# Optimization experiments

Hardware: AMD Instinct MI355X
Metric: run time of the kernel (lower is better)

## Reference

```python
import jax, jax.numpy as jnp
import numpy as np

K = 5  # Chebyshev order


def laplacian(w):
    # normalized Laplacian: I - D^{-1/2} W D^{-1/2}
    d = jnp.sum(w, axis=1)
    d_re = 1.0 / jnp.sqrt(d + 1e-5)
    return jnp.eye(w.shape[0], dtype=w.dtype) - d_re[:, None] * w * d_re[None, :]


def cheb_terms(x, lap, k):
    # x: [B,N,C], lap: [N,N] -> [B,k,N,C]
    # Faithful to torch code: T0 = ones, then (x, lap@x) recurrence for k>2.
    t0 = jnp.ones_like(x)
    if k == 1:
        return t0[:, None]
    t1 = jnp.matmul(lap, x)
    if k == 2:
        return jnp.stack([t0, t1], axis=1)
    terms = [t0, x, t1]
    tkm1, tk = x, t1
    for _ in range(3, k):
        tkm1, tk = tk, 2.0 * jnp.matmul(lap, tk) - tkm1
        terms.append(tk)
    return jnp.stack(terms, axis=1)


def graph_conv(x, lap, w, k):
    # torch: cp.permute(0,2,3,1).flatten(2) @ w, i.e. flat index = c*k + t
    t = cheb_terms(x, lap, k)                       # [B,k,N,C]
    C = x.shape[-1]
    O = w.shape[-1]
    return jnp.einsum('bknc,cko->bno', t, w.reshape(C, k, O))


def setup_inputs() -> dict:
    key = jax.random.key(0)
    ks = jax.random.split(key, 9)
    B, N, Cin, H = 8192, 32, 60, 128
    return {
        'x': jax.random.normal(ks[0], (B, N, Cin), dtype=jnp.float32),
        'adj': jax.random.normal(ks[1], (N, N), dtype=jnp.float32) * 0.1,
        'adj_bias': jax.random.normal(ks[2], (1,), dtype=jnp.float32) * 0.1 + 0.2,
        'w1': jax.random.normal(ks[3], (K * Cin, H), dtype=jnp.float32) * 0.05,
        'b1': jax.random.normal(ks[4], (1, 1, H), dtype=jnp.float32) * 0.05,
        'w2': jax.random.normal(ks[5], (K * H, H), dtype=jnp.float32) * 0.05,
        'b2': jax.random.normal(ks[6], (1, 1, H), dtype=jnp.float32) * 0.05,
        'fc_w': jax.random.normal(ks[7], (2, N * H), dtype=jnp.float32) * 0.02,
        'fc_b': jax.random.normal(ks[8], (2,), dtype=jnp.float32) * 0.02,
    }


def reference(x, adj, adj_bias, w1, b1, w2, b2, fc_w, fc_b):
    # DGCNN.forward (eval mode: dropout = identity)
    a = jax.nn.relu(adj + adj_bias)
    lap = laplacian(a)
    h = graph_conv(x, lap, w1, K)
    h = jax.nn.relu(h + b1)      # B1ReLU
    h = graph_conv(h, lap, w2, K)
    h = jax.nn.relu(h + b2)
    h = h.reshape(h.shape[0], -1)  # [B, N*H]
    return h @ fc_w.T + fc_b
```

## Files before the change

### kernel.cpp

```cpp
#include <hip/hip_runtime.h>

typedef unsigned short u16;
typedef unsigned int u32;
typedef short bf16x8 __attribute__((ext_vector_type(8)));
typedef float f32x4 __attribute__((ext_vector_type(4)));

#define MFMA16(a, b, c) __builtin_amdgcn_mfma_f32_16x16x32_bf16((a), (b), (c), 0, 0, 0)

__device__ __forceinline__ u16 f2bf(float f) {
  u32 u = __builtin_bit_cast(u32, f);
  u += 0x7FFFu + ((u >> 16) & 1u);
  return (u16)(u >> 16);
}
__device__ __forceinline__ u32 pk2bf(float a, float b) {
#if __has_builtin(__builtin_amdgcn_cvt_pk_bf16_f32)
  auto v = __builtin_amdgcn_cvt_pk_bf16_f32(a, b);
  return __builtin_bit_cast(u32, v);
#else
  return (u32)f2bf(a) | ((u32)f2bf(b) << 16);
#endif
}

#define WS_MGF   0
#define WS_WT1F  8192
#define WS_WT2F  73728
#define WS_B1    204800
#define WS_B2    205312

__global__ void prep_kernel(const float* __restrict__ adj,
                            const float* __restrict__ adj_bias,
                            const float* __restrict__ w1,
                            const float* __restrict__ b1,
                            const float* __restrict__ w2,
                            const float* __restrict__ b2,
                            char* __restrict__ ws) {
  const int tid = threadIdx.x;
  if (blockIdx.x == 0) {
    __shared__ float sa[1024], Ls[1024], L2s[1024], L3s[1024], sdre[32];
    float bias = adj_bias[0];
    for (int i = tid; i < 1024; i += 256) sa[i] = fmaxf(adj[i] + bias, 0.0f);
    __syncthreads();
    if (tid < 32) {
      float s = 0.0f;
      for (int c = 0; c < 32; ++c) s += sa[tid * 32 + c];
      sdre[tid] = 1.0f / sqrtf(s + 1e-5f);
    }
    __syncthreads();
    for (int i = tid; i < 1024; i += 256) {
      int n = i >> 5, c = i & 31;
      Ls[i] = (n == c ? 1.0f : 0.0f) - sdre[n] * sa[i] * sdre[c];
    }
    __syncthreads();
    for (int i = tid; i < 1024; i += 256) {
      int r = i >> 5, c = i & 31;
      float s = 0.0f;
      for (int m = 0; m < 32; ++m) s += Ls[r * 32 + m] * Ls[m * 32 + c];
      L2s[i] = s;
    }
    __syncthreads();
    for (int i = tid; i < 1024; i += 256) {
      int r = i >> 5, c = i & 31;
      float s = 0.0f;
      for (int m = 0; m < 32; ++m) s += L2s[r * 32 + m] * Ls[m * 32 + c];
      L3s[i] = s;
    }
    __syncthreads();
    u16* MGf = (u16*)(ws + WS_MGF);
    for (int i = tid; i < 4096; i += 256) {
      int jt = i >> 9, lane = (i >> 3) & 63, j = i & 7;
      int col = jt * 16 + (lane & 15);
      int k = ((lane >> 4) << 3) + j;
      int kk = col >> 5, np = col & 31;
      float v;
      if (kk == 0)      v = (np == k) ? 1.0f : 0.0f;
      else if (kk == 1) v = Ls[np * 32 + k];
      else if (kk == 2) v = 2.0f * L2s[np * 32 + k] - (np == k ? 1.0f : 0.0f);
      else              v = 4.0f * L3s[np * 32 + k] - 3.0f * Ls[np * 32 + k];
      MGf[i] = f2bf(v);
    }
    float* B1 = (float*)(ws + WS_B1);
    float* B2 = (float*)(ws + WS_B2);
    if (tid < 128) {
      float s = b1[tid];
      for (int c = 0; c < 60; ++c) s += w1[(c * 5) * 128 + tid];
      B1[tid] = s;
    } else {
      int o = tid - 128;
      float s = b2[o];
      for (int c = 0; c < 128; ++c) s += w2[(c * 5) * 128 + o];
      B2[o] = s;
    }
  } else {
    u16* WT1F = (u16*)(ws + WS_WT1F);
    u16* WT2F = (u16*)(ws + WS_WT2F);
    int g = (blockIdx.x - 1) * 256 + tid;
    for (int i = g; i < 32768; i += 16 * 256) {
      int ot = i >> 12, ks = (i >> 9) & 7, lane = (i >> 3) & 63, j = i & 7;
      int o = ot * 16 + (lane & 15);
      int kc = ks * 32 + ((lane >> 4) << 3) + j;
      int k = kc >> 6, c = kc & 63;
      WT1F[i] = (c < 60) ? f2bf(w1[(c * 5 + k + 1) * 128 + o]) : (u16)0;
    }
    for (int i = g; i < 65536; i += 16 * 256) {
      int mt = i >> 13, h = (i >> 12) & 1, ks = (i >> 9) & 7;
      int lane = (i >> 3) & 63, j = i & 7;
      int kc = ((ks >> 1) << 7) + ((ks & 1) << 5) + (h << 6) + (((lane >> 4)) << 3) + j;
      int k = kc >> 7, c = kc & 127;
      int o = (mt << 4) + (lane & 15);
      WT2F[i] = f2bf(w2[(c * 5 + k + 1) * 128 + o]);
    }
  }
}

__global__ __launch_bounds__(256, 3) void dgcnn_kernel(
    const float* __restrict__ x,
    const char* __restrict__ ws,
    const float* __restrict__ fc_w,
    const float* __restrict__ fc_b,
    float* __restrict__ out) {
  __shared__ __align__(16) char arena[52224];
  __shared__ float red[16];
  u16* XtA = (u16*)arena;
  u16* XtB = (u16*)(arena + 5120);
  u16* HtA = (u16*)arena;
  u16* HtB = (u16*)(arena + 9216);
  u16* YA  = (u16*)(arena + 18432);
  u16* YB  = (u16*)(arena + 35328);

  const u16* MGf  = (const u16*)(ws + WS_MGF);
  const u16* WT1F = (const u16*)(ws + WS_WT1F);
  const u16* WT2F = (const u16*)(ws + WS_WT2F);
  const float* bias1 = (const float*)(ws + WS_B1);
  const float* bias2 = (const float*)(ws + WS_B2);

  const int tid = threadIdx.x;
  const int w = tid >> 6, lane = tid & 63;
  const int l15 = lane & 15, q = lane >> 4;
  const int b0 = blockIdx.x * 2;
  const f32x4 z4 = {0.0f, 0.0f, 0.0f, 0.0f};

  bf16x8 mB0 = *(const bf16x8*)(MGf + ((2 * w + 0) * 64 + lane) * 8);
  bf16x8 mB1 = *(const bf16x8*)(MGf + ((2 * w + 1) * 64 + lane) * 8);

  for (int i = tid; i < 160; i += 256) {
    int r = 60 + i / 40, c = i % 40;
    XtA[r * 40 + c] = 0;
    XtB[r * 40 + c] = 0;
  }
  const float* xb = x + (size_t)b0 * 1920;
  for (int i = tid; i < 1920; i += 256) {
    int n = i / 60, c = i - n * 60;
    XtA[c * 40 + n] = f2bf(xb[i]);
    XtB[c * 40 + n] = f2bf(xb[1920 + i]);
  }
  __syncthreads();

  {
    f32x4 accA[4][2], accB[4][2];
#pragma unroll
    for (int mt = 0; mt < 4; ++mt) {
      bf16x8 aXA = *(const bf16x8*)&XtA[(mt * 16 + l15) * 40 + q * 8];
      bf16x8 aXB = *(const bf16x8*)&XtB[(mt * 16 + l15) * 40 + q * 8];
      accA[mt][0] = MFMA16(aXA, mB0, z4);
      accA[mt][1] = MFMA16(aXA, mB1, z4);
      accB[mt][0] = MFMA16(aXB, mB0, z4);
      accB[mt][1] = MFMA16(aXB, mB1, z4);
    }
#pragma unroll
    for (int mt = 0; mt < 4; ++mt)
#pragma unroll
      for (int jt = 0; jt < 2; ++jt) {
        int np = jt * 16 + l15;
        int off = np * 264 + w * 64 + mt * 16 + q * 4;
        uint2 vA, vB;
        vA.x = pk2bf(accA[mt][jt][0], accA[mt][jt][1]);
        vA.y = pk2bf(accA[mt][jt][2], accA[mt][jt][3]);
        vB.x = pk2bf(accB[mt][jt][0], accB[mt][jt][1]);
        vB.y = pk2bf(accB[mt][jt][2], accB[mt][jt][3]);
        *(uint2*)&YA[off] = vA;
        *(uint2*)&YB[off] = vB;
      }
  }
  __syncthreads();

  {
    f32x4 accA[2][2] = {{z4, z4}, {z4, z4}};
    f32x4 accB[2][2] = {{z4, z4}, {z4, z4}};
#pragma unroll
    for (int ks = 0; ks < 8; ++ks) {
      bf16x8 wfa = *(const bf16x8*)(WT1F + (((2 * w + 0) * 8 + ks) * 64 + lane) * 8);
      bf16x8 wfb = *(const bf16x8*)(WT1F + (((2 * w + 1) * 8 + ks) * 64 + lane) * 8);
      int offY = ks * 32 + q * 8;
      bf16x8 a0A = *(const bf16x8*)&YA[(l15) * 264 + offY];
      bf16x8 a1A = *(const bf16x8*)&YA[(16 + l15) * 264 + offY];
      bf16x8 a0B = *(const bf16x8*)&YB[(l15) * 264 + offY];
      bf16x8 a1B = *(const bf16x8*)&YB[(16 + l15) * 264 + offY];
      accA[0][0] = MFMA16(a0A, wfa, accA[0][0]);
      accA[0][1] = MFMA16(a0A, wfb, accA[0][1]);
      accA[1][0] = MFMA16(a1A, wfa, accA[1][0]);
      accA[1][1] = MFMA16(a1A, wfb, accA[1][1]);
      accB[0][0] = MFMA16(a0B, wfa, accB[0][0]);
      accB[0][1] = MFMA16(a0B, wfb, accB[0][1]);
      accB[1][0] = MFMA16(a1B, wfa, accB[1][0]);
      accB[1][1] = MFMA16(a1B, wfb, accB[1][1]);
    }
#pragma unroll
    for (int ot = 0; ot < 2; ++ot) {
      int o = (2 * w + ot) * 16 + l15;
      float bv = bias1[o];
#pragma unroll
      for (int mt = 0; mt < 2; ++mt) {
        int off = o * 36 + mt * 16 + q * 4;
        uint2 vA, vB;
        vA.x = pk2bf(fmaxf(accA[mt][ot][0] + bv, 0.0f), fmaxf(accA[mt][ot][1] + bv, 0.0f));
        vA.y = pk2bf(fmaxf(accA[mt][ot][2] + bv, 0.0f), fmaxf(accA[mt][ot][3] + bv, 0.0f));
        vB.x = pk2bf(fmaxf(accB[mt][ot][0] + bv, 0.0f), fmaxf(accB[mt][ot][1] + bv, 0.0f));
        vB.y = pk2bf(fmaxf(accB[mt][ot][2] + bv, 0.0f), fmaxf(accB[mt][ot][3] + bv, 0.0f));
        *(uint2*)&HtA[off] = vA;
        *(uint2*)&HtB[off] = vB;
      }
    }
  }
  __syncthreads();

  f32x4 acc2A[2][2] = {{z4, z4}, {z4, z4}};
  f32x4 acc2B[2][2] = {{z4, z4}, {z4, z4}};
#pragma unroll
  for (int h = 0; h < 2; ++h) {
    bf16x8 wf2[16];
#pragma unroll
    for (int ot = 0; ot < 2; ++ot)
#pragma unroll
      for (int ks = 0; ks < 8; ++ks)
        wf2[ot * 8 + ks] =
            *(const bf16x8*)(WT2F + ((((2 * w + ot) * 2 + h) * 8 + ks) * 64 + lane) * 8);

    {
      f32x4 accA[4][2], accB[4][2];
#pragma unroll
      for (int mtl = 0; mtl < 4; ++mtl) {
        int r = ((4 * h + mtl) * 16 + l15) * 36 + q * 8;
        bf16x8 aHA = *(const bf16x8*)&HtA[r];
        bf16x8 aHB = *(const bf16x8*)&HtB[r];
        accA[mtl][0] = MFMA16(aHA, mB0, z4);
        accA[mtl][1] = MFMA16(aHA, mB1, z4);
        accB[mtl][0] = MFMA16(aHB, mB0, z4);
        accB[mtl][1] = MFMA16(aHB, mB1, z4);
      }
#pragma unroll
      for (int mtl = 0; mtl < 4; ++mtl)
#pragma unroll
        for (int jt = 0; jt < 2; ++jt) {
          int np = jt * 16 + l15;
          int off = np * 264 + w * 64 + mtl * 16 + q * 4;
          uint2 vA, vB;
          vA.x = pk2bf(accA[mtl][jt][0], accA[mtl][jt][1]);
          vA.y = pk2bf(accA[mtl][jt][2], accA[mtl][jt][3]);
          vB.x = pk2bf(accB[mtl][jt][0], accB[mtl][jt][1]);
          vB.y = pk2bf(accB[mtl][jt][2], accB[mtl][jt][3]);
          *(uint2*)&YA[off] = vA;
          *(uint2*)&YB[off] = vB;
        }
    }
    __syncthreads();
#pragma unroll
    for (int ks = 0; ks < 8; ++ks) {
      int offY = ks * 32 + q * 8;
      bf16x8 by0A = *(const bf16x8*)&YA[(l15) * 264 + offY];
      bf16x8 by1A = *(const bf16x8*)&YA[(16 + l15) * 264 + offY];
      bf16x8 by0B = *(const bf16x8*)&YB[(l15) * 264 + offY];
      bf16x8 by1B = *(const bf16x8*)&YB[(16 + l15) * 264 + offY];
      acc2A[0][0] = MFMA16(wf2[ks], by0A, acc2A[0][0]);
      acc2A[0][1] = MFMA16(wf2[ks], by1A, acc2A[0][1]);
      acc2A[1][0] = MFMA16(wf2[8 + ks], by0A, acc2A[1][0]);
      acc2A[1][1] = MFMA16(wf2[8 + ks], by1A, acc2A[1][1]);
      acc2B[0][0] = MFMA16(wf2[ks], by0B, acc2B[0][0]);
      acc2B[0][1] = MFMA16(wf2[ks], by1B, acc2B[0][1]);
      acc2B[1][0] = MFMA16(wf2[8 + ks], by0B, acc2B[1][0]);
      acc2B[1][1] = MFMA16(wf2[8 + ks], by1B, acc2B[1][1]);
    }
    __syncthreads();
  }

  float p0A = 0.0f, p1A = 0.0f, p0B = 0.0f, p1B = 0.0f;
#pragma unroll
  for (int ot = 0; ot < 2; ++ot) {
    int ob = (2 * w + ot) * 16 + q * 4;
    float4 bv = *(const float4*)&bias2[ob];
#pragma unroll
    for (int nt = 0; nt < 2; ++nt) {
      int n = nt * 16 + l15;
      float4 w0 = *(const float4*)&fc_w[n * 128 + ob];
      float4 w1v = *(const float4*)&fc_w[4096 + n * 128 + ob];
      float hA0 = fmaxf(acc2A[ot][nt][0] + bv.x, 0.0f);
      float hA1 = fmaxf(acc2A[ot][nt][1] + bv.y, 0.0f);
      float hA2 = fmaxf(acc2A[ot][nt][2] + bv.z, 0.0f);
      float hA3 = fmaxf(acc2A[ot][nt][3] + bv.w, 0.0f);
      float hB0 = fmaxf(acc2B[ot][nt][0] + bv.x, 0.0f);
      float hB1 = fmaxf(acc2B[ot][nt][1] + bv.y, 0.0f);
      float hB2 = fmaxf(acc2B[ot][nt][2] + bv.z, 0.0f);
      float hB3 = fmaxf(acc2B[ot][nt][3] + bv.w, 0.0f);
      p0A = fmaf(hA0, w0.x, fmaf(hA1, w0.y, fmaf(hA2, w0.z, fmaf(hA3, w0.w, p0A))));
      p1A = fmaf(hA0, w1v.x, fmaf(hA1, w1v.y, fmaf(hA2, w1v.z, fmaf(hA3, w1v.w, p1A))));
      p0B = fmaf(hB0, w0.x, fmaf(hB1, w0.y, fmaf(hB2, w0.z, fmaf(hB3, w0.w, p0B))));
      p1B = fmaf(hB0, w1v.x, fmaf(hB1, w1v.y, fmaf(hB2, w1v.z, fmaf(hB3, w1v.w, p1B))));
    }
  }
#pragma unroll
  for (int off = 32; off >= 1; off >>= 1) {
    p0A += __shfl_xor(p0A, off);
    p1A += __shfl_xor(p1A, off);
    p0B += __shfl_xor(p0B, off);
    p1B += __shfl_xor(p1B, off);
  }
  if (lane == 0) {
    red[w * 4 + 0] = p0A;
    red[w * 4 + 1] = p1A;
    red[w * 4 + 2] = p0B;
    red[w * 4 + 3] = p1B;
  }
  __syncthreads();
  if (tid < 4) {
    float s = red[tid] + red[4 + tid] + red[8 + tid] + red[12 + tid] + fc_b[tid & 1];
    out[(b0 + (tid >> 1)) * 2 + (tid & 1)] = s;
  }
}

extern "C" void kernel_launch(void* const* d_in, const int* in_sizes, int n_in,
                              void* d_out, int out_size, void* d_ws, size_t ws_size,
                              hipStream_t stream) {
  const float* x        = (const float*)d_in[0];
  const float* adj      = (const float*)d_in[1];
  const float* adj_bias = (const float*)d_in[2];
  const float* w1       = (const float*)d_in[3];
  const float* b1       = (const float*)d_in[4];
  const float* w2       = (const float*)d_in[5];
  const float* b2       = (const float*)d_in[6];
  const float* fc_w     = (const float*)d_in[7];
  const float* fc_b     = (const float*)d_in[8];
  float* out = (float*)d_out;
  char* ws   = (char*)d_ws;

  prep_kernel<<<17, 256, 0, stream>>>(adj, adj_bias, w1, b1, w2, b2, ws);
  dgcnn_kernel<<<4096, 256, 0, stream>>>(x, ws, fc_w, fc_b, out);
}
```

Measured before the change: 203.2 us.

## Split Chebyshev stages into smaller channel chunks to shrink LDS and raise occupancy

Both graph-conv layers now process the channel dimension in smaller chunks (2 chunks for layer 1, 4 for layer 2) with a half-width Y staging buffer, and the host-side weight fragments are re-laid out to match. This cuts the LDS arena from about 51KB to 35KB and the launch bound goes from 3 to 4 blocks per SM. Fewer weight registers are live at once (no 16-fragment wf2 array). In exchange there are more barriers per block. The x load also packs both samples with a single conversion.

Result: faster. 192.6 us (-5.2%).

```diff
diff --git a/kernel.cpp b/kernel.cpp
--- a/kernel.cpp
+++ b/kernel.cpp
@@ -95,37 +95,38 @@
     u16* WT2F = (u16*)(ws + WS_WT2F);
     int g = (blockIdx.x - 1) * 256 + tid;
     for (int i = g; i < 32768; i += 16 * 256) {
-      int ot = i >> 12, ks = (i >> 9) & 7, lane = (i >> 3) & 63, j = i & 7;
+      int j = i & 7, lane = (i >> 3) & 63, ks = (i >> 9) & 3;
+      int h = (i >> 11) & 1, ot = i >> 12;
+      int q = lane >> 4;
+      int c = h * 32 + q * 8 + j;
       int o = ot * 16 + (lane & 15);
-      int kc = ks * 32 + ((lane >> 4) << 3) + j;
-      int k = kc >> 6, c = kc & 63;
-      WT1F[i] = (c < 60) ? f2bf(w1[(c * 5 + k + 1) * 128 + o]) : (u16)0;
+      WT1F[i] = (c < 60) ? f2bf(w1[(c * 5 + ks + 1) * 128 + o]) : (u16)0;
     }
     for (int i = g; i < 65536; i += 16 * 256) {
-      int mt = i >> 13, h = (i >> 12) & 1, ks = (i >> 9) & 7;
-      int lane = (i >> 3) & 63, j = i & 7;
-      int kc = ((ks >> 1) << 7) + ((ks & 1) << 5) + (h << 6) + (((lane >> 4)) << 3) + j;
-      int k = kc >> 7, c = kc & 127;
-      int o = (mt << 4) + (lane & 15);
-      WT2F[i] = f2bf(w2[(c * 5 + k + 1) * 128 + o]);
-    }
-  }
-}
-
-__global__ __launch_bounds__(256, 3) void dgcnn_kernel(
+      int j = i & 7, lane = (i >> 3) & 63, ks = (i >> 9) & 3;
+      int h = (i >> 11) & 3, mt = i >> 13;
+      int q = lane >> 4;
+      int c2 = h * 32 + q * 8 + j;
+      int o = mt * 16 + (lane & 15);
+      WT2F[i] = f2bf(w2[(c2 * 5 + ks + 1) * 128 + o]);
+    }
+  }
+}
+
+__global__ __launch_bounds__(256, 4) void dgcnn_kernel(
     const float* __restrict__ x,
     const char* __restrict__ ws,
     const float* __restrict__ fc_w,
     const float* __restrict__ fc_b,
     float* __restrict__ out) {
-  __shared__ __align__(16) char arena[52224];
+  __shared__ __align__(16) char arena[35840];
   __shared__ float red[16];
   u16* XtA = (u16*)arena;
   u16* XtB = (u16*)(arena + 5120);
   u16* HtA = (u16*)arena;
   u16* HtB = (u16*)(arena + 9216);
   u16* YA  = (u16*)(arena + 18432);
-  u16* YB  = (u16*)(arena + 35328);
+  u16* YB  = (u16*)(arena + 27136);
 
   const u16* MGf  = (const u16*)(ws + WS_MGF);
   const u16* WT1F = (const u16*)(ws + WS_WT1F);
@@ -150,136 +151,133 @@
   const float* xb = x + (size_t)b0 * 1920;
   for (int i = tid; i < 1920; i += 256) {
     int n = i / 60, c = i - n * 60;
-    XtA[c * 40 + n] = f2bf(xb[i]);
-    XtB[c * 40 + n] = f2bf(xb[1920 + i]);
+    u32 p = pk2bf(xb[i], xb[1920 + i]);
+    XtA[c * 40 + n] = (u16)p;
+    XtB[c * 40 + n] = (u16)(p >> 16);
   }
   __syncthreads();
 
-  {
-    f32x4 accA[4][2], accB[4][2];
-#pragma unroll
-    for (int mt = 0; mt < 4; ++mt) {
-      bf16x8 aXA = *(const bf16x8*)&XtA[(mt * 16 + l15) * 40 + q * 8];
-      bf16x8 aXB = *(const bf16x8*)&XtB[(mt * 16 + l15) * 40 + q * 8];
-      accA[mt][0] = MFMA16(aXA, mB0, z4);
-      accA[mt][1] = MFMA16(aXA, mB1, z4);
-      accB[mt][0] = MFMA16(aXB, mB0, z4);
-      accB[mt][1] = MFMA16(aXB, mB1, z4);
-    }
-#pragma unroll
-    for (int mt = 0; mt < 4; ++mt)
-#pragma unroll
-      for (int jt = 0; jt < 2; ++jt) {
-        int np = jt * 16 + l15;
-        int off = np * 264 + w * 64 + mt * 16 + q * 4;
-        uint2 vA, vB;
-        vA.x = pk2bf(accA[mt][jt][0], accA[mt][jt][1]);
-        vA.y = pk2bf(accA[mt][jt][2], accA[mt][jt][3]);
-        vB.x = pk2bf(accB[mt][jt][0], accB[mt][jt][1]);
-        vB.y = pk2bf(accB[mt][jt][2], accB[mt][jt][3]);
-        *(uint2*)&YA[off] = vA;
-        *(uint2*)&YB[off] = vB;
+  f32x4 acc1A[2][2] = {{z4, z4}, {z4, z4}};
+  f32x4 acc1B[2][2] = {{z4, z4}, {z4, z4}};
+#pragma unroll
+  for (int h = 0; h < 2; ++h) {
+    {
+      f32x4 gA[2][2], gB[2][2];
+#pragma unroll
+      for (int mtl = 0; mtl < 2; ++mtl) {
+        int roff = ((2 * h + mtl) * 16 + l15) * 40 + q * 8;
+        bf16x8 aA = *(const bf16x8*)&XtA[roff];
+        bf16x8 aB = *(const bf16x8*)&XtB[roff];
+        gA[mtl][0] = MFMA16(aA, mB0, z4);
+        gA[mtl][1] = MFMA16(aA, mB1, z4);
+        gB[mtl][0] = MFMA16(aB, mB0, z4);
+        gB[mtl][1] = MFMA16(aB, mB1, z4);
       }
-  }
-  __syncthreads();
-
-  {
-    f32x4 accA[2][2] = {{z4, z4}, {z4, z4}};
-    f32x4 accB[2][2] = {{z4, z4}, {z4, z4}};
-#pragma unroll
-    for (int ks = 0; ks < 8; ++ks) {
-      bf16x8 wfa = *(const bf16x8*)(WT1F + (((2 * w + 0) * 8 + ks) * 64 + lane) * 8);
-      bf16x8 wfb = *(const bf16x8*)(WT1F + (((2 * w + 1) * 8 + ks) * 64 + lane) * 8);
-      int offY = ks * 32 + q * 8;
-      bf16x8 a0A = *(const bf16x8*)&YA[(l15) * 264 + offY];
-      bf16x8 a1A = *(const bf16x8*)&YA[(16 + l15) * 264 + offY];
-      bf16x8 a0B = *(const bf16x8*)&YB[(l15) * 264 + offY];
-      bf16x8 a1B = *(const bf16x8*)&YB[(16 + l15) * 264 + offY];
-      accA[0][0] = MFMA16(a0A, wfa, accA[0][0]);
-      accA[0][1] = MFMA16(a0A, wfb, accA[0][1]);
-      accA[1][0] = MFMA16(a1A, wfa, accA[1][0]);
-      accA[1][1] = MFMA16(a1A, wfb, accA[1][1]);
-      accB[0][0] = MFMA16(a0B, wfa, accB[0][0]);
-      accB[0][1] = MFMA16(a0B, wfb, accB[0][1]);
-      accB[1][0] = MFMA16(a1B, wfa, accB[1][0]);
-      accB[1][1] = MFMA16(a1B, wfb, accB[1][1]);
-    }
-#pragma unroll
-    for (int ot = 0; ot < 2; ++ot) {
-      int o = (2 * w + ot) * 16 + l15;
-      float bv = bias1[o];
-#pragma unroll
-      for (int mt = 0; mt < 2; ++mt) {
-        int off = o * 36 + mt * 16 + q * 4;
-        uint2 vA, vB;
-        vA.x = pk2bf(fmaxf(accA[mt][ot][0] + bv, 0.0f), fmaxf(accA[mt][ot][1] + bv, 0.0f));
-        vA.y = pk2bf(fmaxf(accA[mt][ot][2] + bv, 0.0f), fmaxf(accA[mt][ot][3] + bv, 0.0f));
-        vB.x = pk2bf(fmaxf(accB[mt][ot][0] + bv, 0.0f), fmaxf(accB[mt][ot][1] + bv, 0.0f));
-        vB.y = pk2bf(fmaxf(accB[mt][ot][2] + bv, 0.0f), fmaxf(accB[mt][ot][3] + bv, 0.0f));
-        *(uint2*)&HtA[off] = vA;
-        *(uint2*)&HtB[off] = vB;
-      }
-    }
-  }
-  __syncthreads();
-
-  f32x4 acc2A[2][2] = {{z4, z4}, {z4, z4}};
-  f32x4 acc2B[2][2] = {{z4, z4}, {z4, z4}};
-#pragma unroll
-  for (int h = 0; h < 2; ++h) {
-    bf16x8 wf2[16];
-#pragma unroll
-    for (int ot = 0; ot < 2; ++ot)
-#pragma unroll
-      for (int ks = 0; ks < 8; ++ks)
-        wf2[ot * 8 + ks] =
-            *(const bf16x8*)(WT2F + ((((2 * w + ot) * 2 + h) * 8 + ks) * 64 + lane) * 8);
-
-    {
-      f32x4 accA[4][2], accB[4][2];
-#pragma unroll
-      for (int mtl = 0; mtl < 4; ++mtl) {
-        int r = ((4 * h + mtl) * 16 + l15) * 36 + q * 8;
-        bf16x8 aHA = *(const bf16x8*)&HtA[r];
-        bf16x8 aHB = *(const bf16x8*)&HtB[r];
-        accA[mtl][0] = MFMA16(aHA, mB0, z4);
-        accA[mtl][1] = MFMA16(aHA, mB1, z4);
-        accB[mtl][0] = MFMA16(aHB, mB0, z4);
-        accB[mtl][1] = MFMA16(aHB, mB1, z4);
-      }
-#pragma unroll
-      for (int mtl = 0; mtl < 4; ++mtl)
-#pragma unroll
-        for (int jt = 0; jt < 2; ++jt) {
-          int np = jt * 16 + l15;
-          int off = np * 264 + w * 64 + mtl * 16 + q * 4;
+#pragma unroll
+      for (int mtl = 0; mtl < 2; ++mtl)
+#pragma unroll
+        for (int jtl = 0; jtl < 2; ++jtl) {
+          int np = jtl * 16 + l15;
+          int off = np * 136 + w * 32 + mtl * 16 + q * 4;
           uint2 vA, vB;
-          vA.x = pk2bf(accA[mtl][jt][0], accA[mtl][jt][1]);
-          vA.y = pk2bf(accA[mtl][jt][2], accA[mtl][jt][3]);
-          vB.x = pk2bf(accB[mtl][jt][0], accB[mtl][jt][1]);
-          vB.y = pk2bf(accB[mtl][jt][2], accB[mtl][jt][3]);
+          vA.x = pk2bf(gA[mtl][jtl][0], gA[mtl][jtl][1]);
+          vA.y = pk2bf(gA[mtl][jtl][2], gA[mtl][jtl][3]);
+          vB.x = pk2bf(gB[mtl][jtl][0], gB[mtl][jtl][1]);
+          vB.y = pk2bf(gB[mtl][jtl][2], gB[mtl][jtl][3]);
           *(uint2*)&YA[off] = vA;
           *(uint2*)&YB[off] = vB;
         }
     }
     __syncthreads();
 #pragma unroll
-    for (int ks = 0; ks < 8; ++ks) {
-      int offY = ks * 32 + q * 8;
-      bf16x8 by0A = *(const bf16x8*)&YA[(l15) * 264 + offY];
-      bf16x8 by1A = *(const bf16x8*)&YA[(16 + l15) * 264 + offY];
-      bf16x8 by0B = *(const bf16x8*)&YB[(l15) * 264 + offY];
-      bf16x8 by1B = *(const bf16x8*)&YB[(16 + l15) * 264 + offY];
-      acc2A[0][0] = MFMA16(wf2[ks], by0A, acc2A[0][0]);
-      acc2A[0][1] = MFMA16(wf2[ks], by1A, acc2A[0][1]);
-      acc2A[1][0] = MFMA16(wf2[8 + ks], by0A, acc2A[1][0]);
-      acc2A[1][1] = MFMA16(wf2[8 + ks], by1A, acc2A[1][1]);
-      acc2B[0][0] = MFMA16(wf2[ks], by0B, acc2B[0][0]);
-      acc2B[0][1] = MFMA16(wf2[ks], by1B, acc2B[0][1]);
-      acc2B[1][0] = MFMA16(wf2[8 + ks], by0B, acc2B[1][0]);
-      acc2B[1][1] = MFMA16(wf2[8 + ks], by1B, acc2B[1][1]);
-    }
-    __syncthreads();
+    for (int ks = 0; ks < 4; ++ks) {
+      bf16x8 wfa = *(const bf16x8*)(WT1F + ((((2 * w + 0) * 2 + h) * 4 + ks) * 64 + lane) * 8);
+      bf16x8 wfb = *(const bf16x8*)(WT1F + ((((2 * w + 1) * 2 + h) * 4 + ks) * 64 + lane) * 8);
+      int yoff = ks * 32 + q * 8;
+      bf16x8 a0A = *(const bf16x8*)&YA[l15 * 136 + yoff];
+      bf16x8 a1A = *(const bf16x8*)&YA[(16 + l15) * 136 + yoff];
+      bf16x8 a0B = *(const bf16x8*)&YB[l15 * 136 + yoff];
+      bf16x8 a1B = *(const bf16x8*)&YB[(16 + l15) * 136 + yoff];
+      acc1A[0][0] = MFMA16(a0A, wfa, acc1A[0][0]);
+      acc1A[0][1] = MFMA16(a0A, wfb, acc1A[0][1]);
+      acc1A[1][0] = MFMA16(a1A, wfa, acc1A[1][0]);
+      acc1A[1][1] = MFMA16(a1A, wfb, acc1A[1][1]);
+      acc1B[0][0] = MFMA16(a0B, wfa, acc1B[0][0]);
+      acc1B[0][1] = MFMA16(a0B, wfb, acc1B[0][1]);
+      acc1B[1][0] = MFMA16(a1B, wfa, acc1B[1][0]);
+      acc1B[1][1] = MFMA16(a1B, wfb, acc1B[1][1]);
+    }
+    if (h == 0) __syncthreads();
+  }
+#pragma unroll
+  for (int ot = 0; ot < 2; ++ot) {
+    int o = (2 * w + ot) * 16 + l15;
+    float bv = bias1[o];
+#pragma unroll
+    for (int mt = 0; mt < 2; ++mt) {
+      int off = o * 36 + mt * 16 + q * 4;
+      uint2 vA, vB;
+      vA.x = pk2bf(fmaxf(acc1A[mt][ot][0] + bv, 0.0f), fmaxf(acc1A[mt][ot][1] + bv, 0.0f));
+      vA.y = pk2bf(fmaxf(acc1A[mt][ot][2] + bv, 0.0f), fmaxf(acc1A[mt][ot][3] + bv, 0.0f));
+      vB.x = pk2bf(fmaxf(acc1B[mt][ot][0] + bv, 0.0f), fmaxf(acc1B[mt][ot][1] + bv, 0.0f));
+      vB.y = pk2bf(fmaxf(acc1B[mt][ot][2] + bv, 0.0f), fmaxf(acc1B[mt][ot][3] + bv, 0.0f));
+      *(uint2*)&HtA[off] = vA;
+      *(uint2*)&HtB[off] = vB;
+    }
+  }
+  __syncthreads();
+
+  f32x4 acc2A[2][2] = {{z4, z4}, {z4, z4}};
+  f32x4 acc2B[2][2] = {{z4, z4}, {z4, z4}};
+#pragma unroll
+  for (int h = 0; h < 4; ++h) {
+    {
+      f32x4 gA[2][2], gB[2][2];
+#pragma unroll
+      for (int mtl = 0; mtl < 2; ++mtl) {
+        int roff = ((2 * h + mtl) * 16 + l15) * 36 + q * 8;
+        bf16x8 aA = *(const bf16x8*)&HtA[roff];
+        bf16x8 aB = *(const bf16x8*)&HtB[roff];
+        gA[mtl][0] = MFMA16(aA, mB0, z4);
+        gA[mtl][1] = MFMA16(aA, mB1, z4);
+        gB[mtl][0] = MFMA16(aB, mB0, z4);
+        gB[mtl][1] = MFMA16(aB, mB1, z4);
+      }
+#pragma unroll
+      for (int mtl = 0; mtl < 2; ++mtl)
+#pragma unroll
+        for (int jtl = 0; jtl < 2; ++jtl) {
+          int np = jtl * 16 + l15;
+          int off = np * 136 + w * 32 + mtl * 16 + q * 4;
+          uint2 vA, vB;
+          vA.x = pk2bf(gA[mtl][jtl][0], gA[mtl][jtl][1]);
+          vA.y = pk2bf(gA[mtl][jtl][2], gA[mtl][jtl][3]);
+          vB.x = pk2bf(gB[mtl][jtl][0], gB[mtl][jtl][1]);
+          vB.y = pk2bf(gB[mtl][jtl][2], gB[mtl][jtl][3]);
+          *(uint2*)&YA[off] = vA;
+          *(uint2*)&YB[off] = vB;
+        }
+    }
+    __syncthreads();
+#pragma unroll
+    for (int ks = 0; ks < 4; ++ks) {
+      bf16x8 wfa = *(const bf16x8*)(WT2F + ((((2 * w + 0) * 4 + h) * 4 + ks) * 64 + lane) * 8);
+      bf16x8 wfb = *(const bf16x8*)(WT2F + ((((2 * w + 1) * 4 + h) * 4 + ks) * 64 + lane) * 8);
+      int yoff = ks * 32 + q * 8;
+      bf16x8 by0A = *(const bf16x8*)&YA[l15 * 136 + yoff];
+      bf16x8 by1A = *(const bf16x8*)&YA[(16 + l15) * 136 + yoff];
+      bf16x8 by0B = *(const bf16x8*)&YB[l15 * 136 + yoff];
+      bf16x8 by1B = *(const bf16x8*)&YB[(16 + l15) * 136 + yoff];
+      acc2A[0][0] = MFMA16(wfa, by0A, acc2A[0][0]);
+      acc2A[0][1] = MFMA16(wfa, by1A, acc2A[0][1]);
+      acc2A[1][0] = MFMA16(wfb, by0A, acc2A[1][0]);
+      acc2A[1][1] = MFMA16(wfb, by1A, acc2A[1][1]);
+      acc2B[0][0] = MFMA16(wfa, by0B, acc2B[0][0]);
+      acc2B[0][1] = MFMA16(wfa, by1B, acc2B[0][1]);
+      acc2B[1][0] = MFMA16(wfb, by0B, acc2B[1][0]);
+      acc2B[1][1] = MFMA16(wfb, by1B, acc2B[1][1]);
+    }
+    if (h < 3) __syncthreads();
   }
 
   float p0A = 0.0f, p1A = 0.0f, p0B = 0.0f, p1B = 0.0f;
```
